# Kernel optimization log

Hardware: AMD Instinct MI355X
Metric: run time of the kernel (lower is better)

The kernel has to match this reference:

```python
import jax, jax.numpy as jnp
import numpy as np

N = 16384        # tokens (batch*seq)
D_MODEL = 4096
D_HALF = D_MODEL // 2
NUM_EXPERTS = 64
TOP_K = 4
SCALE = 2.0


def setup_inputs() -> dict:
    key = jax.random.key(0)
    k_u, k_ex, k_ey = jax.random.split(key, 3)
    u = jax.random.normal(k_u, (N, D_MODEL), dtype=jnp.float32)
    E_x = jax.random.normal(k_ex, (D_HALF, NUM_EXPERTS), dtype=jnp.float32) * 0.01
    E_y = jax.random.normal(k_ey, (D_HALF, NUM_EXPERTS), dtype=jnp.float32) * 0.01
    bias = jnp.zeros((NUM_EXPERTS,), dtype=jnp.float32)
    # torus-shape scalar parameters (torch init values)
    c = jnp.float32(2.0)
    d = jnp.float32(2.0)
    a1 = jnp.float32(4.0)
    b1 = jnp.float32(4.0)
    return {"u": u, "E_x": E_x, "E_y": E_y, "bias": bias,
            "c": c, "d": d, "a1": a1, "b1": b1, "top_k": TOP_K}


def reference(u, E_x, E_y, bias, c, d, a1, b1, top_k):
    d_half = E_x.shape[0]
    num_experts = E_x.shape[1]
    # dual small GEMM + tanh squash onto [-scale, scale]
    x = jnp.tanh(u[..., :d_half] @ E_x) * SCALE        # [N, E]
    y = jnp.tanh(u[..., d_half:] @ E_y) * SCALE        # [N, E]
    xa, ya = jnp.abs(x), jnp.abs(y)
    # 4CM torus: f(x,y) = (|x|^a1 + |y|^b1) * exp(-(|x|^c + |y|^d))
    scores = (xa ** a1 + ya ** b1) * jnp.exp(-(xa ** c + ya ** d)) + bias
    topk_s, topk_i = jax.lax.top_k(scores, top_k)       # [N, k]
    probs = jax.nn.softmax(scores, axis=-1)             # [N, E]
    aux_loss = jnp.sum(jnp.mean(probs, axis=0) ** 2) * num_experts
    return topk_i, topk_s, scores, aux_loss
```

## Files before the change

kernel.cpp:

```cpp
#include <hip/hip_runtime.h>
#include <math.h>
#include <stdint.h>

#define N_TOK 16384
#define DM    4096
#define DH    2048
#define NE    64
#define TBK   32
#define TOPK  4
#define KQ    1024
#define NSTEP 32

#define OFF_TI  0
#define OFF_TS  (N_TOK * TOPK)
#define OFF_SC  (N_TOK * TOPK * 2)
#define OFF_AUX (N_TOK * TOPK * 2 + N_TOK * NE)

typedef __attribute__((ext_vector_type(4)))  float  f32x4;
typedef __attribute__((ext_vector_type(16))) float  f32x16;
typedef __attribute__((ext_vector_type(8)))  __bf16 bf16x8;
typedef __attribute__((ext_vector_type(8)))  unsigned short u16x8;

#define BSPLIT_ELEMS (2 * 64 * 3 * 2 * 2 * 64 * 8)

__device__ __forceinline__ void split3(float a, __bf16& h, __bf16& m, __bf16& l) {
    h = (__bf16)a;
    float r = a - (float)h;
    m = (__bf16)r;
    float r2 = r - (float)m;
    l = (__bf16)r2;
}

__device__ __forceinline__ void stage16(const float* g, void* l) {
    __builtin_amdgcn_global_load_lds(
        (const __attribute__((address_space(1))) unsigned int*)(uintptr_t)g,
        (__attribute__((address_space(3))) unsigned int*)(uintptr_t)l,
        16, 0, 0);
}

__global__ __launch_bounds__(256) void prep_B(
    const float* __restrict__ Ex, const float* __restrict__ Ey,
    __bf16* __restrict__ Bws)
{
    const int t    = blockIdx.x * 256 + threadIdx.x;
    const int lane = t & 63;
    const int sk   = (t >> 6) & 1;
    const int et   = (t >> 7) & 1;
    const int ks   = (t >> 8) & 63;
    const int h    = (t >> 14) & 1;
    const float* E = h ? Ey : Ex;
    const int e  = et * 32 + (lane & 31);
    const int k0 = ks * 32 + sk * 16 + (lane >> 5) * 8;
    bf16x8 vh, vm, vl;
    #pragma unroll
    for (int j = 0; j < 8; ++j) {
        __bf16 hh, mm, ll;
        split3(E[(size_t)(k0 + j) * NE + e], hh, mm, ll);
        vh[j] = hh; vm[j] = mm; vl[j] = ll;
    }
    #pragma unroll
    for (int s = 0; s < 3; ++s) {
        size_t base = ((((((size_t)h * 64 + ks) * 3 + s) * 2 + et) * 2 + sk) * 64 + lane) * 8;
        *(bf16x8*)(Bws + base) = (s == 0) ? vh : (s == 1) ? vm : vl;
    }
}

__global__ __launch_bounds__(256, 2) void torus_mfma(
    const float* __restrict__ u, const __bf16* __restrict__ Bws,
    const float* __restrict__ bias,
    const float* __restrict__ cp, const float* __restrict__ dp,
    const float* __restrict__ a1p, const float* __restrict__ b1p,
    float* __restrict__ out, float* __restrict__ esum)
{
    __shared__ __align__(16) unsigned char smem[65536];

    const int tid  = threadIdx.x;
    const int t0   = blockIdx.x * TBK;
    const int lane = tid & 63;
    const int wv   = tid >> 6;
    const int h    = wv >> 1;
    const int kh   = wv & 1;
    const int lr   = lane & 31;
    const int lkh  = lane >> 5;

    float* ring = (float*)(smem + wv * 16384);

    const int   srow  = lane >> 3;
    const int   schk  = (lane & 7) ^ srow;
    const float* gbase = u + (size_t)(t0 + srow) * DM + h * DH + kh * KQ + schk * 4;

    auto stage = [&](int s) {
        const float* g = gbase + s * 32;
        unsigned char* lb = (unsigned char*)ring + (s & 3) * 4096;
        #pragma unroll
        for (int i = 0; i < 4; ++i)
            stage16(g + (size_t)i * 8 * DM, lb + i * 1024);
    };

    int rb[4];
    {
        const int ch0 = 2 * lkh, ch1 = 2 * lkh + 1, ch2 = 4 + 2 * lkh, ch3 = 5 + 2 * lkh;
        rb[0] = lr * 32 + ((ch0 ^ (lr & 7)) * 4);
        rb[1] = lr * 32 + ((ch1 ^ (lr & 7)) * 4);
        rb[2] = lr * 32 + ((ch2 ^ (lr & 7)) * 4);
        rb[3] = lr * 32 + ((ch3 ^ (lr & 7)) * 4);
    }

    const __bf16* bp0 = Bws + ((size_t)h * 64 + kh * 32) * 6144 + lane * 8;
    auto loadB = [&](bf16x8 (&b)[12], int s) {
        const __bf16* bp = bp0 + (size_t)s * 6144;
        #pragma unroll
        for (int et = 0; et < 2; ++et)
            #pragma unroll
            for (int sk = 0; sk < 2; ++sk) {
                b[0 + et * 2 + sk] = *(const bf16x8*)(bp + (0 + et * 2 + sk) * 512);
                b[4 + et * 2 + sk] = *(const bf16x8*)(bp + (4 + et * 2 + sk) * 512);
                b[8 + et * 2 + sk] = *(const bf16x8*)(bp + (8 + et * 2 + sk) * 512);
            }
    };

    f32x16 acc[2][2] = {};

    auto body = [&](int s, bf16x8 (&bu)[12], bf16x8 (&bn)[12]) {
        const int sn = (s + 1 < NSTEP) ? s + 1 : s;
        loadB(bn, sn);
        if (s + 3 < NSTEP) stage(s + 3);
        __builtin_amdgcn_sched_barrier(0);
        asm volatile("s_waitcnt vmcnt(36)" ::: "memory");
        __builtin_amdgcn_sched_barrier(0);
        const float* rp = ring + (s & 3) * 1024;
        f32x4 r0 = *(const f32x4*)(rp + rb[0]);
        f32x4 r1 = *(const f32x4*)(rp + rb[1]);
        f32x4 r2 = *(const f32x4*)(rp + rb[2]);
        f32x4 r3 = *(const f32x4*)(rp + rb[3]);
        u16x8 sh[2], sm[2], sl[2];
        #pragma unroll
        for (int q = 0; q < 2; ++q)
            #pragma unroll
            for (int j = 0; j < 4; ++j) {
                {
                    float a = (q == 0 ? r0 : r1)[j];
                    unsigned h32 = __float_as_uint(a) & 0xFFFF0000u;
                    float rr = a - __uint_as_float(h32);
                    unsigned m32 = __float_as_uint(rr) & 0xFFFF0000u;
                    float r2f = rr - __uint_as_float(m32);
                    sh[0][q * 4 + j] = (unsigned short)(h32 >> 16);
                    sm[0][q * 4 + j] = (unsigned short)(m32 >> 16);
                    sl[0][q * 4 + j] = (unsigned short)(__float_as_uint(r2f) >> 16);
                }
                {
                    float a = (q == 0 ? r2 : r3)[j];
                    unsigned h32 = __float_as_uint(a) & 0xFFFF0000u;
                    float rr = a - __uint_as_float(h32);
                    unsigned m32 = __float_as_uint(rr) & 0xFFFF0000u;
                    float r2f = rr - __uint_as_float(m32);
                    sh[1][q * 4 + j] = (unsigned short)(h32 >> 16);
                    sm[1][q * 4 + j] = (unsigned short)(m32 >> 16);
                    sl[1][q * 4 + j] = (unsigned short)(__float_as_uint(r2f) >> 16);
                }
            }
        __builtin_amdgcn_sched_barrier(0);
        #pragma unroll
        for (int et = 0; et < 2; ++et)
            #pragma unroll
            for (int sk = 0; sk < 2; ++sk) {
                bf16x8 vh_ = __builtin_bit_cast(bf16x8, sh[sk]);
                bf16x8 vm_ = __builtin_bit_cast(bf16x8, sm[sk]);
                bf16x8 vl_ = __builtin_bit_cast(bf16x8, sl[sk]);
                acc[sk][et] = __builtin_amdgcn_mfma_f32_32x32x16_bf16(vh_, bu[0 + et * 2 + sk], acc[sk][et], 0, 0, 0);
                acc[sk][et] = __builtin_amdgcn_mfma_f32_32x32x16_bf16(vm_, bu[0 + et * 2 + sk], acc[sk][et], 0, 0, 0);
                acc[sk][et] = __builtin_amdgcn_mfma_f32_32x32x16_bf16(vl_, bu[0 + et * 2 + sk], acc[sk][et], 0, 0, 0);
            }
        #pragma unroll
        for (int et = 0; et < 2; ++et)
            #pragma unroll
            for (int sk = 0; sk < 2; ++sk) {
                bf16x8 vh_ = __builtin_bit_cast(bf16x8, sh[sk]);
                bf16x8 vm_ = __builtin_bit_cast(bf16x8, sm[sk]);
                acc[sk][et] = __builtin_amdgcn_mfma_f32_32x32x16_bf16(vh_, bu[4 + et * 2 + sk], acc[sk][et], 0, 0, 0);
                acc[sk][et] = __builtin_amdgcn_mfma_f32_32x32x16_bf16(vm_, bu[4 + et * 2 + sk], acc[sk][et], 0, 0, 0);
            }
        #pragma unroll
        for (int et = 0; et < 2; ++et)
            #pragma unroll
            for (int sk = 0; sk < 2; ++sk) {
                bf16x8 vh_ = __builtin_bit_cast(bf16x8, sh[sk]);
                acc[sk][et] = __builtin_amdgcn_mfma_f32_32x32x16_bf16(vh_, bu[8 + et * 2 + sk], acc[sk][et], 0, 0, 0);
            }
        __builtin_amdgcn_sched_barrier(0);
    };

    stage(0); stage(1); stage(2);
    bf16x8 b0[12], b1[12];
    loadB(b0, 0);
    #pragma unroll 1
    for (int s = 0; s < NSTEP; s += 2) {
        body(s,     b0, b1);
        body(s + 1, b1, b0);
    }

    __syncthreads();
    float (*pre)[NE][36]   = (float(*)[NE][36])smem;
    float (*stile)[NE + 1] = (float(*)[NE + 1])(smem + 18432);
    float* s_m  = (float*)(smem + 18432 + 8320);
    float* s_inv = s_m + TBK;

    if (kh == 0) {
        #pragma unroll
        for (int et = 0; et < 2; ++et) {
            f32x16 a = acc[0][et] + acc[1][et];
            #pragma unroll
            for (int q = 0; q < 4; ++q) {
                int e  = et * 32 + lr;
                int tk = q * 8 + 4 * lkh;
                f32x4 v = { a[q*4+0], a[q*4+1], a[q*4+2], a[q*4+3] };
                *(f32x4*)&pre[h][e][tk] = v;
            }
        }
    }
    __syncthreads();
    if (kh == 1) {
        #pragma unroll
        for (int et = 0; et < 2; ++et) {
            f32x16 a = acc[0][et] + acc[1][et];
            #pragma unroll
            for (int q = 0; q < 4; ++q) {
                int e  = et * 32 + lr;
                int tk = q * 8 + 4 * lkh;
                f32x4 v = { a[q*4+0], a[q*4+1], a[q*4+2], a[q*4+3] };
                f32x4 o = *(f32x4*)&pre[h][e][tk];
                v += o;
                *(f32x4*)&pre[h][e][tk] = v;
            }
        }
    }
    __syncthreads();

    {
        const float c_ = *cp, d_ = *dp, a1_ = *a1p, b1_ = *b1p;
        const int tk = tid & 31;
        const int e0 = (tid >> 5) * 8;
        #pragma unroll
        for (int i = 0; i < 8; ++i) {
            int e = e0 + i;
            float x = pre[0][e][tk];
            float y = pre[1][e][tk];
            x = tanhf(x) * 2.0f; y = tanhf(y) * 2.0f;
            float xa = fabsf(x), ya = fabsf(y);
            float sc = (powf(xa, a1_) + powf(ya, b1_)) *
                       expf(-(powf(xa, c_) + powf(ya, d_))) + bias[e];
            stile[tk][e] = sc;
        }
    }
    __syncthreads();

    if (tid < TBK) {
        const int t = tid;
        float bv[TOPK]; int bi[TOPK];
        #pragma unroll
        for (int p = 0; p < TOPK; ++p) {
            float best = -INFINITY; int besti = 0;
            for (int e = 0; e < NE; ++e) {
                float v = stile[t][e];
                bool taken = false;
                #pragma unroll
                for (int q = 0; q < p; ++q) taken = taken || (bi[q] == e);
                if (!taken && v > best) { best = v; besti = e; }
            }
            bv[p] = best; bi[p] = besti;
        }
        const float m = bv[0];
        float denom = 0.0f;
        for (int e = 0; e < NE; ++e) denom += expf(stile[t][e] - m);
        const float inv = 1.0f / denom;
        s_m[t] = m; s_inv[t] = inv;
        #pragma unroll
        for (int p = 0; p < TOPK; ++p) {
            out[OFF_TI + (size_t)(t0 + t) * TOPK + p] = (float)bi[p];
            out[OFF_TS + (size_t)(t0 + t) * TOPK + p] = bv[p];
        }
    }
    __syncthreads();

    if (tid < NE) {
        const int e = tid;
        float cs = 0.0f;
        for (int t = 0; t < TBK; ++t)
            cs += expf(stile[t][e] - s_m[t]) * s_inv[t];
        atomicAdd(&esum[e], cs);
    }

    for (int idx = tid; idx < TBK * NE; idx += 256)
        out[OFF_SC + (size_t)t0 * NE + idx] = stile[idx >> 6][idx & (NE - 1)];
}

__global__ __launch_bounds__(64) void torus_aux(const float* __restrict__ esum,
                                                float* __restrict__ out)
{
    const int e = threadIdx.x;
    float s = esum[e] * (1.0f / (float)N_TOK);
    float v = s * s;
    #pragma unroll
    for (int off = 32; off > 0; off >>= 1) v += __shfl_down(v, off);
    if (e == 0) out[OFF_AUX] = v * (float)NE;
}

extern "C" void kernel_launch(void* const* d_in, const int* in_sizes, int n_in,
                              void* d_out, int out_size, void* d_ws, size_t ws_size,
                              hipStream_t stream) {
    const float* u    = (const float*)d_in[0];
    const float* Ex   = (const float*)d_in[1];
    const float* Ey   = (const float*)d_in[2];
    const float* bias = (const float*)d_in[3];
    const float* cp   = (const float*)d_in[4];
    const float* dp   = (const float*)d_in[5];
    const float* a1p  = (const float*)d_in[6];
    const float* b1p  = (const float*)d_in[7];
    float* out = (float*)d_out;
    __bf16* Bws = (__bf16*)d_ws;
    float* esum = (float*)((char*)d_ws + (size_t)BSPLIT_ELEMS * sizeof(__bf16));

    prep_B<<<128, 256, 0, stream>>>(Ex, Ey, Bws);
    hipMemsetAsync(esum, 0, NE * sizeof(float), stream);
    torus_mfma<<<N_TOK / TBK, 256, 0, stream>>>(u, Bws, bias, cp, dp, a1p, b1p, out, esum);
    torus_aux<<<1, 64, 0, stream>>>(esum, out);
}
```

Baseline: 109.2 us.

## Split MFMA work across 16 waves with expert-half sharing of staged tiles

Grows the block from 4 to 16 waves. Each wave now handles one expert half (et), one quarter of K and one of the x/y halves. Pairs of waves share a double-buffered LDS ring that only the et==0 wave fills, with s_barrier synchronisation per step, and the per-wave register footprint (accumulators, B fragments) is cut in half. The partial sums are reduced in LDS across the four K quarters in the epilogue. The aim is more latency hiding per CU and less redundant loading of u. The cost is block-wide barriers each step and a shallower prefetch depth.

```diff
diff --git a/kernel.cpp b/kernel.cpp
--- a/kernel.cpp
+++ b/kernel.cpp
@@ -8,8 +8,8 @@
 #define NE    64
 #define TBK   32
 #define TOPK  4
-#define KQ    1024
-#define NSTEP 32
+#define KQ4   512
+#define NSTEP 16
 
 #define OFF_TI  0
 #define OFF_TS  (N_TOK * TOPK)
@@ -65,7 +65,7 @@
     }
 }
 
-__global__ __launch_bounds__(256, 2) void torus_mfma(
+__global__ __launch_bounds__(1024, 1) void torus_mfma(
     const float* __restrict__ u, const __bf16* __restrict__ Bws,
     const float* __restrict__ bias,
     const float* __restrict__ cp, const float* __restrict__ dp,
@@ -73,25 +73,28 @@
     float* __restrict__ out, float* __restrict__ esum)
 {
     __shared__ __align__(16) unsigned char smem[65536];
+    __shared__ float stile[TBK][NE + 1];
+    __shared__ float s_m[TBK], s_inv[TBK];
 
     const int tid  = threadIdx.x;
     const int t0   = blockIdx.x * TBK;
     const int lane = tid & 63;
     const int wv   = tid >> 6;
-    const int h    = wv >> 1;
-    const int kh   = wv & 1;
+    const int et   = wv & 1;
+    const int kq   = (wv >> 1) & 3;
+    const int h    = wv >> 3;
     const int lr   = lane & 31;
     const int lkh  = lane >> 5;
 
-    float* ring = (float*)(smem + wv * 16384);
+    unsigned char* ring = smem + (wv >> 1) * 8192;
 
     const int   srow  = lane >> 3;
     const int   schk  = (lane & 7) ^ srow;
-    const float* gbase = u + (size_t)(t0 + srow) * DM + h * DH + kh * KQ + schk * 4;
+    const float* gbase = u + (size_t)(t0 + srow) * DM + h * DH + kq * KQ4 + schk * 4;
 
     auto stage = [&](int s) {
         const float* g = gbase + s * 32;
-        unsigned char* lb = (unsigned char*)ring + (s & 3) * 4096;
+        unsigned char* lb = ring + (s & 1) * 4096;
         #pragma unroll
         for (int i = 0; i < 4; ++i)
             stage16(g + (size_t)i * 8 * DM, lb + i * 1024);
@@ -99,40 +102,43 @@
 
     int rb[4];
     {
-        const int ch0 = 2 * lkh, ch1 = 2 * lkh + 1, ch2 = 4 + 2 * lkh, ch3 = 5 + 2 * lkh;
-        rb[0] = lr * 32 + ((ch0 ^ (lr & 7)) * 4);
-        rb[1] = lr * 32 + ((ch1 ^ (lr & 7)) * 4);
-        rb[2] = lr * 32 + ((ch2 ^ (lr & 7)) * 4);
-        rb[3] = lr * 32 + ((ch3 ^ (lr & 7)) * 4);
-    }
-
-    const __bf16* bp0 = Bws + ((size_t)h * 64 + kh * 32) * 6144 + lane * 8;
-    auto loadB = [&](bf16x8 (&b)[12], int s) {
+        const int c0 = 2 * lkh, c1 = 2 * lkh + 1, c2 = 4 + 2 * lkh, c3 = 5 + 2 * lkh;
+        rb[0] = lr * 32 + ((c0 ^ (lr & 7)) * 4);
+        rb[1] = lr * 32 + ((c1 ^ (lr & 7)) * 4);
+        rb[2] = lr * 32 + ((c2 ^ (lr & 7)) * 4);
+        rb[3] = lr * 32 + ((c3 ^ (lr & 7)) * 4);
+    }
+
+    const __bf16* bp0 = Bws + ((size_t)h * 64 + kq * 16) * 6144 + lane * 8;
+    auto loadB = [&](bf16x8 (&b)[6], int s) {
         const __bf16* bp = bp0 + (size_t)s * 6144;
         #pragma unroll
-        for (int et = 0; et < 2; ++et)
+        for (int sp = 0; sp < 3; ++sp)
             #pragma unroll
-            for (int sk = 0; sk < 2; ++sk) {
-                b[0 + et * 2 + sk] = *(const bf16x8*)(bp + (0 + et * 2 + sk) * 512);
-                b[4 + et * 2 + sk] = *(const bf16x8*)(bp + (4 + et * 2 + sk) * 512);
-                b[8 + et * 2 + sk] = *(const bf16x8*)(bp + (8 + et * 2 + sk) * 512);
-            }
+            for (int sk = 0; sk < 2; ++sk)
+                b[sp * 2 + sk] = *(const bf16x8*)(bp + (sp * 4 + et * 2 + sk) * 512);
     };
 
-    f32x16 acc[2][2] = {};
-
-    auto body = [&](int s, bf16x8 (&bu)[12], bf16x8 (&bn)[12]) {
+    f32x16 acc[2] = {};
+
+    auto body = [&](int s, bf16x8 (&bu)[6], bf16x8 (&bn)[6]) {
         const int sn = (s + 1 < NSTEP) ? s + 1 : s;
         loadB(bn, sn);
-        if (s + 3 < NSTEP) stage(s + 3);
-        __builtin_amdgcn_sched_barrier(0);
-        asm volatile("s_waitcnt vmcnt(36)" ::: "memory");
-        __builtin_amdgcn_sched_barrier(0);
-        const float* rp = ring + (s & 3) * 1024;
+        __builtin_amdgcn_sched_barrier(0);
+        if (et == 0)
+            asm volatile("s_waitcnt vmcnt(16)" ::: "memory");
+        __builtin_amdgcn_sched_barrier(0);
+        __builtin_amdgcn_s_barrier();
+        const float* rp = (const float*)(ring + (s & 1) * 4096);
         f32x4 r0 = *(const f32x4*)(rp + rb[0]);
         f32x4 r1 = *(const f32x4*)(rp + rb[1]);
         f32x4 r2 = *(const f32x4*)(rp + rb[2]);
         f32x4 r3 = *(const f32x4*)(rp + rb[3]);
+        asm volatile("s_waitcnt lgkmcnt(0)" ::: "memory");
+        __builtin_amdgcn_sched_barrier(0);
+        __builtin_amdgcn_s_barrier();
+        if (et == 0 && s + 2 < NSTEP) stage(s + 2);
+        __builtin_amdgcn_sched_barrier(0);
         u16x8 sh[2], sm[2], sl[2];
         #pragma unroll
         for (int q = 0; q < 2; ++q)
@@ -161,37 +167,22 @@
             }
         __builtin_amdgcn_sched_barrier(0);
         #pragma unroll
-        for (int et = 0; et < 2; ++et)
-            #pragma unroll
-            for (int sk = 0; sk < 2; ++sk) {
-                bf16x8 vh_ = __builtin_bit_cast(bf16x8, sh[sk]);
-                bf16x8 vm_ = __builtin_bit_cast(bf16x8, sm[sk]);
-                bf16x8 vl_ = __builtin_bit_cast(bf16x8, sl[sk]);
-                acc[sk][et] = __builtin_amdgcn_mfma_f32_32x32x16_bf16(vh_, bu[0 + et * 2 + sk], acc[sk][et], 0, 0, 0);
-                acc[sk][et] = __builtin_amdgcn_mfma_f32_32x32x16_bf16(vm_, bu[0 + et * 2 + sk], acc[sk][et], 0, 0, 0);
-                acc[sk][et] = __builtin_amdgcn_mfma_f32_32x32x16_bf16(vl_, bu[0 + et * 2 + sk], acc[sk][et], 0, 0, 0);
-            }
-        #pragma unroll
-        for (int et = 0; et < 2; ++et)
-            #pragma unroll
-            for (int sk = 0; sk < 2; ++sk) {
-                bf16x8 vh_ = __builtin_bit_cast(bf16x8, sh[sk]);
-                bf16x8 vm_ = __builtin_bit_cast(bf16x8, sm[sk]);
-                acc[sk][et] = __builtin_amdgcn_mfma_f32_32x32x16_bf16(vh_, bu[4 + et * 2 + sk], acc[sk][et], 0, 0, 0);
-                acc[sk][et] = __builtin_amdgcn_mfma_f32_32x32x16_bf16(vm_, bu[4 + et * 2 + sk], acc[sk][et], 0, 0, 0);
-            }
-        #pragma unroll
-        for (int et = 0; et < 2; ++et)
-            #pragma unroll
-            for (int sk = 0; sk < 2; ++sk) {
-                bf16x8 vh_ = __builtin_bit_cast(bf16x8, sh[sk]);
-                acc[sk][et] = __builtin_amdgcn_mfma_f32_32x32x16_bf16(vh_, bu[8 + et * 2 + sk], acc[sk][et], 0, 0, 0);
-            }
+        for (int sk = 0; sk < 2; ++sk) {
+            bf16x8 vh_ = __builtin_bit_cast(bf16x8, sh[sk]);
+            bf16x8 vm_ = __builtin_bit_cast(bf16x8, sm[sk]);
+            bf16x8 vl_ = __builtin_bit_cast(bf16x8, sl[sk]);
+            acc[sk] = __builtin_amdgcn_mfma_f32_32x32x16_bf16(vh_, bu[0 + sk], acc[sk], 0, 0, 0);
+            acc[sk] = __builtin_amdgcn_mfma_f32_32x32x16_bf16(vm_, bu[0 + sk], acc[sk], 0, 0, 0);
+            acc[sk] = __builtin_amdgcn_mfma_f32_32x32x16_bf16(vl_, bu[0 + sk], acc[sk], 0, 0, 0);
+            acc[sk] = __builtin_amdgcn_mfma_f32_32x32x16_bf16(vh_, bu[2 + sk], acc[sk], 0, 0, 0);
+            acc[sk] = __builtin_amdgcn_mfma_f32_32x32x16_bf16(vm_, bu[2 + sk], acc[sk], 0, 0, 0);
+            acc[sk] = __builtin_amdgcn_mfma_f32_32x32x16_bf16(vh_, bu[4 + sk], acc[sk], 0, 0, 0);
+        }
         __builtin_amdgcn_sched_barrier(0);
     };
 
-    stage(0); stage(1); stage(2);
-    bf16x8 b0[12], b1[12];
+    if (et == 0) { stage(0); stage(1); }
+    bf16x8 b0[6], b1[6];
     loadB(b0, 0);
     #pragma unroll 1
     for (int s = 0; s < NSTEP; s += 2) {
@@ -200,56 +191,36 @@
     }
 
     __syncthreads();
-    float (*pre)[NE][36]   = (float(*)[NE][36])smem;
-    float (*stile)[NE + 1] = (float(*)[NE + 1])(smem + 18432);
-    float* s_m  = (float*)(smem + 18432 + 8320);
-    float* s_inv = s_m + TBK;
-
-    if (kh == 0) {
-        #pragma unroll
-        for (int et = 0; et < 2; ++et) {
-            f32x16 a = acc[0][et] + acc[1][et];
+    float (*part)[TBK][32] = (float(*)[TBK][32])smem;
+    {
+        f32x16 a = acc[0] + acc[1];
+        #pragma unroll
+        for (int q = 0; q < 4; ++q)
             #pragma unroll
-            for (int q = 0; q < 4; ++q) {
-                int e  = et * 32 + lr;
-                int tk = q * 8 + 4 * lkh;
-                f32x4 v = { a[q*4+0], a[q*4+1], a[q*4+2], a[q*4+3] };
-                *(f32x4*)&pre[h][e][tk] = v;
+            for (int j = 0; j < 4; ++j) {
+                int row = q * 8 + 4 * lkh + j;
+                part[wv][row][lr] = a[q * 4 + j];
             }
-        }
-    }
-    __syncthreads();
-    if (kh == 1) {
-        #pragma unroll
-        for (int et = 0; et < 2; ++et) {
-            f32x16 a = acc[0][et] + acc[1][et];
-            #pragma unroll
-            for (int q = 0; q < 4; ++q) {
-                int e  = et * 32 + lr;
-                int tk = q * 8 + 4 * lkh;
-                f32x4 v = { a[q*4+0], a[q*4+1], a[q*4+2], a[q*4+3] };
-                f32x4 o = *(f32x4*)&pre[h][e][tk];
-                v += o;
-                *(f32x4*)&pre[h][e][tk] = v;
-            }
-        }
     }
     __syncthreads();
 
     {
         const float c_ = *cp, d_ = *dp, a1_ = *a1p, b1_ = *b1p;
-        const int tk = tid & 31;
-        const int e0 = (tid >> 5) * 8;
-        #pragma unroll
-        for (int i = 0; i < 8; ++i) {
-            int e = e0 + i;
-            float x = pre[0][e][tk];
-            float y = pre[1][e][tk];
+        #pragma unroll
+        for (int it = 0; it < 2; ++it) {
+            int idx = tid + it * 1024;
+            int t   = idx & 31;
+            int e   = idx >> 5;
+            int eh  = e >> 5, ec = e & 31;
+            float x = part[0 + 0 * 2 + eh][t][ec] + part[0 + 1 * 2 + eh][t][ec]
+                    + part[0 + 2 * 2 + eh][t][ec] + part[0 + 3 * 2 + eh][t][ec];
+            float y = part[8 + 0 * 2 + eh][t][ec] + part[8 + 1 * 2 + eh][t][ec]
+                    + part[8 + 2 * 2 + eh][t][ec] + part[8 + 3 * 2 + eh][t][ec];
             x = tanhf(x) * 2.0f; y = tanhf(y) * 2.0f;
             float xa = fabsf(x), ya = fabsf(y);
             float sc = (powf(xa, a1_) + powf(ya, b1_)) *
                        expf(-(powf(xa, c_) + powf(ya, d_))) + bias[e];
-            stile[tk][e] = sc;
+            stile[t][e] = sc;
         }
     }
     __syncthreads();
@@ -290,8 +261,12 @@
         atomicAdd(&esum[e], cs);
     }
 
-    for (int idx = tid; idx < TBK * NE; idx += 256)
+    if (tid < TBK * NE - 1024 || tid < 1024) {
+        int idx = tid;
         out[OFF_SC + (size_t)t0 * NE + idx] = stile[idx >> 6][idx & (NE - 1)];
+        idx = tid + 1024;
+        out[OFF_SC + (size_t)t0 * NE + idx] = stile[idx >> 6][idx & (NE - 1)];
+    }
 }
 
 __global__ __launch_bounds__(64) void torus_aux(const float* __restrict__ esum,
@@ -322,6 +297,6 @@
 
     prep_B<<<128, 256, 0, stream>>>(Ex, Ey, Bws);
     hipMemsetAsync(esum, 0, NE * sizeof(float), stream);
-    torus_mfma<<<N_TOK / TBK, 256, 0, stream>>>(u, Bws, bias, cp, dp, a1p, b1p, out, esum);
+    torus_mfma<<<N_TOK / TBK, 1024, 0, stream>>>(u, Bws, bias, cp, dp, a1p, b1p, out, esum);
     torus_aux<<<1, 64, 0, stream>>>(esum, out);
 }
```

After: 261.6 us. 2.4x slower.
